# Kernel tuning notes

Measured on AMD Instinct MI355X. Metric: run time of the kernel, lower is better.

## Reference

```python
import jax, jax.numpy as jnp
import numpy as np

D_MODEL = 1024
NUM_HEADS = 16
D_K = D_MODEL // NUM_HEADS
B, S = 2, 2048


def setup_inputs() -> dict:
    key = jax.random.key(0)
    ks = jax.random.split(key, 12)
    s = 1.0 / np.sqrt(D_MODEL)
    inp = {
        "Q": jax.random.normal(ks[0], (B, S, D_MODEL), jnp.float32),
        "K": jax.random.normal(ks[1], (B, S, D_MODEL), jnp.float32),
        "V": jax.random.normal(ks[2], (B, S, D_MODEL), jnp.float32),
        "mask": jnp.tril(jnp.ones((S, S), jnp.int32))[None, None],  # causal [1,1,S,S]
        "W_Q": jax.random.uniform(ks[3], (D_MODEL, D_MODEL), jnp.float32, -s, s),
        "b_Q": jax.random.uniform(ks[4], (D_MODEL,), jnp.float32, -s, s),
        "W_K": jax.random.uniform(ks[5], (D_MODEL, D_MODEL), jnp.float32, -s, s),
        "b_K": jax.random.uniform(ks[6], (D_MODEL,), jnp.float32, -s, s),
        "W_V": jax.random.uniform(ks[7], (D_MODEL, D_MODEL), jnp.float32, -s, s),
        "b_V": jax.random.uniform(ks[8], (D_MODEL,), jnp.float32, -s, s),
        "W_O": jax.random.uniform(ks[9], (D_MODEL, D_MODEL), jnp.float32, -s, s),
        "b_O": jax.random.uniform(ks[10], (D_MODEL,), jnp.float32, -s, s),
    }
    return inp


def _split_heads(x):
    b, s, _ = x.shape
    return x.reshape(b, s, NUM_HEADS, D_K).transpose(0, 2, 1, 3)  # [B,H,S,d_k]


def reference(Q, K, V, mask, W_Q, b_Q, W_K, b_K, W_V, b_V, W_O, b_O):
    q = _split_heads(Q @ W_Q.T + b_Q)
    k = _split_heads(K @ W_K.T + b_K)
    v = _split_heads(V @ W_V.T + b_V)
    scores = jnp.einsum("bhqd,bhkd->bhqk", q, k) / jnp.sqrt(jnp.float32(D_K))
    scores = jnp.where(mask == 0, -jnp.inf, scores)
    attn = jax.nn.softmax(scores, axis=-1)
    out = jnp.einsum("bhqk,bhkd->bhqd", attn, v)
    out = out.transpose(0, 2, 1, 3).reshape(Q.shape[0], Q.shape[1], D_MODEL)
    out = out @ W_O.T + b_O
    return out, attn
```

## Files before the change

### kernel.cpp

```cpp
#include <hip/hip_runtime.h>

typedef __attribute__((ext_vector_type(4))) float f32x4;
typedef __attribute__((ext_vector_type(8))) __bf16 bf16x8;
typedef __attribute__((ext_vector_type(4))) __bf16 bf16x4;

#define D_MODEL 1024
#define S_LEN 2048
#define MROWS 4096

#if __has_builtin(__builtin_amdgcn_exp2f)
#define EXP2F(x) __builtin_amdgcn_exp2f(x)
#else
#define EXP2F(x) exp2f(x)
#endif
#if __has_builtin(__builtin_amdgcn_logf)
#define LOG2F(x) __builtin_amdgcn_logf(x)
#else
#define LOG2F(x) log2f(x)
#endif

#define QSCALE 0.1803368801111204f

__device__ __forceinline__ void gload_lds16(const void* g, void* l) {
  __builtin_amdgcn_global_load_lds(
      (const __attribute__((address_space(1))) unsigned int*)g,
      (__attribute__((address_space(3))) unsigned int*)l, 16, 0, 0);
}

__global__ void cvt_qkv(const float* __restrict__ Q, const float* __restrict__ K,
                        const float* __restrict__ V, __bf16* __restrict__ dst) {
  const int y = blockIdx.y;
  const float* src = (y == 0) ? Q : (y == 1) ? K : V;
  __bf16* d = dst + (size_t)y * (MROWS * D_MODEL);
  const int n4 = MROWS * D_MODEL / 4;
  for (int i = blockIdx.x * blockDim.x + threadIdx.x; i < n4; i += 512 * 256) {
    f32x4 v = *(const f32x4*)(src + i * 4);
    bf16x4 o;
#pragma unroll
    for (int j = 0; j < 4; ++j) o[j] = (__bf16)v[j];
    *(bf16x4*)(d + i * 4) = o;
  }
}

__global__ void cvt_w(const float* __restrict__ w0, const float* __restrict__ w1,
                      const float* __restrict__ w2, const float* __restrict__ w3,
                      __bf16* __restrict__ dst) {
  const int y = blockIdx.y;
  const float* src = (y == 0) ? w0 : (y == 1) ? w1 : (y == 2) ? w2 : w3;
  const float sc = (y == 0) ? QSCALE : 1.0f;
  __bf16* d = dst + (size_t)y * (D_MODEL * D_MODEL);
  const int n4 = D_MODEL * D_MODEL / 4;
  for (int i = blockIdx.x * blockDim.x + threadIdx.x; i < n4; i += 256 * 256) {
    f32x4 v = *(const f32x4*)(src + i * 4);
    bf16x4 o;
#pragma unroll
    for (int j = 0; j < 4; ++j) o[j] = (__bf16)(v[j] * sc);
    *(bf16x4*)(d + i * 4) = o;
  }
}

__device__ __forceinline__ void gemm_core64(const __bf16* __restrict__ A,
                                            const __bf16* __restrict__ B,
                                            __bf16* As, __bf16* Bs,
                                            int m0, int n0, f32x4 (&acc)[4][4]) {
  const int tid = threadIdx.x;
  const int lane = tid & 63, wid = tid >> 6;
  const int li = lane & 15, g = lane >> 4;
  const int wr = wid >> 1, wc = wid & 1;
  const int srow = tid >> 3, sc = tid & 7;
  const int scol = (sc ^ (srow & 7)) * 8;
  const int sw = li & 7;
  for (int k0 = 0; k0 < D_MODEL; k0 += 64) {
#pragma unroll
    for (int i = 0; i < 4; ++i) {
      const int r = i * 32 + srow;
      gload_lds16(A + (size_t)(m0 + r) * D_MODEL + k0 + scol, (char*)As + i * 4096 + wid * 1024);
      gload_lds16(B + (size_t)(n0 + r) * D_MODEL + k0 + scol, (char*)Bs + i * 4096 + wid * 1024);
    }
    __syncthreads();
#pragma unroll
    for (int kk = 0; kk < 2; ++kk) {
      bf16x8 af[4], bfr[4];
#pragma unroll
      for (int i = 0; i < 4; ++i) {
        af[i]  = *(const bf16x8*)&As[(wr * 64 + i * 16 + li) * 64 + (((kk * 4 + g) ^ sw) * 8)];
        bfr[i] = *(const bf16x8*)&Bs[(wc * 64 + i * 16 + li) * 64 + (((kk * 4 + g) ^ sw) * 8)];
      }
      __builtin_amdgcn_s_setprio(1);
#pragma unroll
      for (int i = 0; i < 4; ++i)
#pragma unroll
        for (int j = 0; j < 4; ++j)
          acc[i][j] = __builtin_amdgcn_mfma_f32_16x16x32_bf16(af[i], bfr[j], acc[i][j], 0, 0, 0);
      __builtin_amdgcn_s_setprio(0);
    }
    __syncthreads();
  }
}

__global__ __launch_bounds__(256) void qkv_gemm(
    const __bf16* __restrict__ Qb, const __bf16* __restrict__ Kb, const __bf16* __restrict__ Vb,
    const __bf16* __restrict__ Wq, const __bf16* __restrict__ Wk, const __bf16* __restrict__ Wv,
    const float* __restrict__ bq, const float* __restrict__ bk, const float* __restrict__ bv,
    __bf16* __restrict__ qp, __bf16* __restrict__ kp, __bf16* __restrict__ vt) {
  __shared__ __bf16 As[128 * 64];
  __shared__ __bf16 Bs[128 * 64];
  const int z = blockIdx.z;
  const __bf16* A = (z == 0) ? Qb : (z == 1) ? Kb : Vb;
  const __bf16* B = (z == 0) ? Wq : (z == 1) ? Wk : Wv;
  const float* bias = (z == 0) ? bq : (z == 1) ? bk : bv;
  const float bsc = (z == 0) ? QSCALE : 1.0f;
  const int m0 = blockIdx.x * 128, n0 = blockIdx.y * 128;
  f32x4 acc[4][4] = {};
  gemm_core64(A, B, As, Bs, m0, n0, acc);

  const int lane = threadIdx.x & 63, wid = threadIdx.x >> 6;
  const int li = lane & 15, g = lane >> 4;
  const int wr = wid >> 1, wc = wid & 1;
#pragma unroll
  for (int j = 0; j < 4; ++j) {
    const int n = n0 + wc * 64 + j * 16 + li;
    const float bv_ = bias[n] * bsc;
#pragma unroll
    for (int i = 0; i < 4; ++i) {
#pragma unroll
      for (int r = 0; r < 4; ++r) {
        const int m = m0 + wr * 64 + i * 16 + g * 4 + r;
        const float v = acc[i][j][r] + bv_;
        if (z == 2) {
          const int bb = m >> 11, s = m & 2047;
          vt[((size_t)(bb * D_MODEL + n)) * S_LEN + s] = (__bf16)v;
        } else {
          __bf16* o = (z == 0) ? qp : kp;
          o[(size_t)m * D_MODEL + n] = (__bf16)v;
        }
      }
    }
  }
}

__global__ __launch_bounds__(256) void o_gemm(const __bf16* __restrict__ ctx,
                                              const __bf16* __restrict__ Wo,
                                              const float* __restrict__ bo,
                                              float* __restrict__ out) {
  __shared__ __bf16 As[128 * 64];
  __shared__ __bf16 Bs[128 * 64];
  const int m0 = blockIdx.x * 128, n0 = blockIdx.y * 128;
  f32x4 acc[4][4] = {};
  gemm_core64(ctx, Wo, As, Bs, m0, n0, acc);

  const int lane = threadIdx.x & 63, wid = threadIdx.x >> 6;
  const int li = lane & 15, g = lane >> 4;
  const int wr = wid >> 1, wc = wid & 1;
#pragma unroll
  for (int j = 0; j < 4; ++j) {
    const int n = n0 + wc * 64 + j * 16 + li;
    const float bv_ = bo[n];
#pragma unroll
    for (int i = 0; i < 4; ++i)
#pragma unroll
      for (int r = 0; r < 4; ++r) {
        const int m = m0 + wr * 64 + i * 16 + g * 4 + r;
        out[(size_t)m * D_MODEL + n] = acc[i][j][r] + bv_;
      }
  }
}

__global__ __launch_bounds__(256) void attn_fused2(const __bf16* __restrict__ qp,
                                                   const __bf16* __restrict__ kp,
                                                   const __bf16* __restrict__ vt,
                                                   float* __restrict__ attn,
                                                   __bf16* __restrict__ ctx) {
  const int bid = blockIdx.x;
  const int qt = 31 - (bid >> 5);
  const int bh = bid & 31;
  const int b = bh >> 4, h = bh & 15;
  const int tid = threadIdx.x, lane = tid & 63, wid = tid >> 6;
  const int li = lane & 15, g = lane >> 4;
  const int sw = li & 7;
  const int qrow0 = qt * 64 + wid * 16;
  const float NEG_INF = -__builtin_inff();

  __shared__ __bf16 k_lds[2][64 * 64];
  __shared__ __bf16 v_lds[2][64 * 64];
  __shared__ __bf16 p_lds[4][16 * 64];

  const __bf16* qbase = qp + ((size_t)(b * S_LEN + qrow0 + li)) * D_MODEL + h * 64 + g * 8;
  const bf16x8 qf0 = *(const bf16x8*)qbase;
  const bf16x8 qf1 = *(const bf16x8*)(qbase + 32);

  const int srow = tid >> 3;
  const int sc = tid & 7;
  const int schunk = (sc ^ (srow & 7)) * 8;
  const __bf16* kpb = kp + (size_t)(b * S_LEN) * D_MODEL + h * 64 + schunk;
  const __bf16* vpb = vt + (size_t)(bh * 64) * S_LEN + schunk;

  auto stage_k = [&](int kt, int bufi) {
#pragma unroll
    for (int i = 0; i < 2; ++i)
      gload_lds16(kpb + (size_t)(kt * 64 + i * 32 + srow) * D_MODEL,
                  (char*)k_lds[bufi] + i * 4096 + wid * 1024);
  };
  auto stage_v = [&](int kt, int bufi) {
#pragma unroll
    for (int i = 0; i < 2; ++i)
      gload_lds16(vpb + (size_t)(i * 32 + srow) * S_LEN + kt * 64,
                  (char*)v_lds[bufi] + i * 4096 + wid * 1024);
  };
  auto qk_tile = [&](const __bf16* kb, f32x4 (&sv)[4]) {
    __builtin_amdgcn_s_setprio(1);
#pragma unroll
    for (int sub = 0; sub < 4; ++sub) {
      const __bf16* rp = kb + (sub * 16 + li) * 64;
      const bf16x8 k0 = *(const bf16x8*)(rp + ((g ^ sw) * 8));
      const bf16x8 k1 = *(const bf16x8*)(rp + (((4 + g) ^ sw) * 8));
      f32x4 t = {};
      t = __builtin_amdgcn_mfma_f32_16x16x32_bf16(qf0, k0, t, 0, 0, 0);
      t = __builtin_amdgcn_mfma_f32_16x16x32_bf16(qf1, k1, t, 0, 0, 0);
      sv[sub] = t;
    }
    __builtin_amdgcn_s_setprio(0);
  };

  float m_[4], l_[4];
#pragma unroll
  for (int r = 0; r < 4; ++r) { m_[r] = NEG_INF; l_[r] = 0.f; }

  int buf = 0;
  stage_k(0, 0);
  for (int kt = 0; kt <= qt; ++kt) {
    __syncthreads();
    stage_k(kt + 1, buf ^ 1);
    f32x4 sv[4];
    qk_tile(k_lds[buf], sv);
    if (kt == qt) {
      const int rowl = wid * 16 + g * 4;
#pragma unroll
      for (int sub = 0; sub < 4; ++sub) {
        const int coll = sub * 16 + li;
#pragma unroll
        for (int r = 0; r < 4; ++r)
          if (coll > rowl + r) sv[sub][r] = NEG_INF;
      }
    }
#pragma unroll
    for (int r = 0; r < 4; ++r) {
      const float v0 = sv[0][r], v1 = sv[1][r], v2 = sv[2][r], v3 = sv[3][r];
      float tm = fmaxf(fmaxf(v0, v1), fmaxf(v2, v3));
      tm = fmaxf(tm, __shfl_xor(tm, 1));
      tm = fmaxf(tm, __shfl_xor(tm, 2));
      tm = fmaxf(tm, __shfl_xor(tm, 4));
      tm = fmaxf(tm, __shfl_xor(tm, 8));
      const float mn = fmaxf(m_[r], tm);
      float e = (EXP2F(v0 - mn) + EXP2F(v1 - mn)) + (EXP2F(v2 - mn) + EXP2F(v3 - mn));
      e += __shfl_xor(e, 1);
      e += __shfl_xor(e, 2);
      e += __shfl_xor(e, 4);
      e += __shfl_xor(e, 8);
      l_[r] = l_[r] * EXP2F(m_[r] - mn) + e;
      m_[r] = mn;
    }
    buf ^= 1;
  }

  float c_[4];
#pragma unroll
  for (int r = 0; r < 4; ++r) c_[r] = m_[r] + LOG2F(l_[r]);

  float* attn_bh = attn + (size_t)bh * S_LEN * S_LEN;
  float* arp[4];
#pragma unroll
  for (int r = 0; r < 4; ++r)
    arp[r] = attn_bh + (size_t)(qrow0 + g * 4 + r) * S_LEN + li;

  __bf16* pw = &p_lds[wid][0];
  f32x4 acc[4] = {};

  __syncthreads();
  buf = 0;
  stage_k(0, 0);
  stage_v(0, 0);
  for (int kt = 0; kt <= qt; ++kt) {
    __syncthreads();
    stage_k(kt + 1, buf ^ 1);
    stage_v(kt + 1, buf ^ 1);
    f32x4 sv[4];
    qk_tile(k_lds[buf], sv);
    if (kt == qt) {
      const int rowl = wid * 16 + g * 4;
#pragma unroll
      for (int sub = 0; sub < 4; ++sub) {
        const int coll = sub * 16 + li;
#pragma unroll
        for (int r = 0; r < 4; ++r)
          if (coll > rowl + r) sv[sub][r] = NEG_INF;
      }
    }
    const int colbase = kt * 64;
#pragma unroll
    for (int r = 0; r < 4; ++r) {
      const int prow = g * 4 + r;
#pragma unroll
      for (int sub = 0; sub < 4; ++sub) {
        const float p = EXP2F(sv[sub][r] - c_[r]);
        arp[r][colbase + sub * 16] = p;
        pw[prow * 64 + (((sub * 2 + (li >> 3)) ^ (prow & 7)) * 8) + (li & 7)] = (__bf16)p;
      }
    }
    __builtin_amdgcn_s_setprio(1);
    const bf16x8 pa0 = *(const bf16x8*)&pw[li * 64 + ((g ^ sw) * 8)];
    const bf16x8 pa1 = *(const bf16x8*)&pw[li * 64 + (((4 + g) ^ sw) * 8)];
    const __bf16* vb = v_lds[buf];
#pragma unroll
    for (int c4 = 0; c4 < 4; ++c4) {
      const __bf16* vrp = vb + (c4 * 16 + li) * 64;
      const bf16x8 vf0 = *(const bf16x8*)(vrp + ((g ^ sw) * 8));
      const bf16x8 vf1 = *(const bf16x8*)(vrp + (((4 + g) ^ sw) * 8));
      acc[c4] = __builtin_amdgcn_mfma_f32_16x16x32_bf16(pa0, vf0, acc[c4], 0, 0, 0);
      acc[c4] = __builtin_amdgcn_mfma_f32_16x16x32_bf16(pa1, vf1, acc[c4], 0, 0, 0);
    }
    __builtin_amdgcn_s_setprio(0);
    buf ^= 1;
  }

#pragma unroll
  for (int c4 = 0; c4 < 4; ++c4)
#pragma unroll
    for (int r = 0; r < 4; ++r)
      ctx[((size_t)(b * S_LEN) + qrow0 + g * 4 + r) * D_MODEL + h * 64 + c4 * 16 + li] =
          (__bf16)acc[c4][r];

  const int c0 = (qt + 1) * 64;
  for (int r = 0; r < 16; ++r) {
    float* rowp = attn_bh + (size_t)(qrow0 + r) * S_LEN;
    for (int col = c0 + lane * 4; col < S_LEN; col += 256) {
      f32x4 z = {};
      *(f32x4*)(rowp + col) = z;
    }
  }
}

extern "C" void kernel_launch(void* const* d_in, const int* in_sizes, int n_in,
                              void* d_out, int out_size, void* d_ws, size_t ws_size,
                              hipStream_t stream) {
  const float* Q  = (const float*)d_in[0];
  const float* K  = (const float*)d_in[1];
  const float* V  = (const float*)d_in[2];
  const float* W_Q = (const float*)d_in[4];
  const float* b_Q = (const float*)d_in[5];
  const float* W_K = (const float*)d_in[6];
  const float* b_K = (const float*)d_in[7];
  const float* W_V = (const float*)d_in[8];
  const float* b_V = (const float*)d_in[9];
  const float* W_O = (const float*)d_in[10];
  const float* b_O = (const float*)d_in[11];

  char* ws = (char*)d_ws;
  __bf16* Qb  = (__bf16*)(ws + 0);
  __bf16* Wq  = (__bf16*)(ws + 25165824);
  __bf16* qp  = (__bf16*)(ws + 33554432);
  __bf16* kp  = (__bf16*)(ws + 41943040);
  __bf16* vtb = (__bf16*)(ws + 50331648);
  __bf16* ctx = (__bf16*)(ws + 58720256);
  __bf16* Kb = Qb + (size_t)MROWS * D_MODEL;
  __bf16* Vb = Kb + (size_t)MROWS * D_MODEL;
  __bf16* Wk = Wq + (size_t)D_MODEL * D_MODEL;
  __bf16* Wv = Wk + (size_t)D_MODEL * D_MODEL;
  __bf16* Wo = Wv + (size_t)D_MODEL * D_MODEL;

  float* out = (float*)d_out;
  float* attn = out + (size_t)MROWS * D_MODEL;

  cvt_qkv<<<dim3(512, 3), 256, 0, stream>>>(Q, K, V, Qb);
  cvt_w<<<dim3(256, 4), 256, 0, stream>>>(W_Q, W_K, W_V, W_O, Wq);

  qkv_gemm<<<dim3(32, 8, 3), 256, 0, stream>>>(Qb, Kb, Vb, Wq, Wk, Wv,
                                               b_Q, b_K, b_V, qp, kp, vtb);

  attn_fused2<<<1024, 256, 0, stream>>>(qp, kp, vtb, attn, ctx);

  o_gemm<<<dim3(32, 8), 256, 0, stream>>>(ctx, Wo, b_O, out);
}
```

Before: 247.6 us.

## Transpose score tiles per lane and drop online max in fused attention

Swaps the MFMA operands in the QK product so that each lane owns one query row and four consecutive key columns. Probabilities can then be written to the attention output as contiguous float4 stores and to LDS as bf16x4 chunks, with a new swizzle for the P buffer. The first pass drops the running max and rescaling and just sums exp2 of the raw scores, needing only two cross-lane shuffles, then multiplies by the reciprocal sum in the second pass. This removes shuffle-heavy reductions and scattered scalar stores. The cost is that softmax without max subtraction can overflow or lose precision when scores are large.

```diff
diff --git a/kernel.cpp b/kernel.cpp
--- a/kernel.cpp
+++ b/kernel.cpp
@@ -12,11 +12,6 @@
 #define EXP2F(x) __builtin_amdgcn_exp2f(x)
 #else
 #define EXP2F(x) exp2f(x)
-#endif
-#if __has_builtin(__builtin_amdgcn_logf)
-#define LOG2F(x) __builtin_amdgcn_logf(x)
-#else
-#define LOG2F(x) log2f(x)
 #endif
 
 #define QSCALE 0.1803368801111204f
@@ -166,7 +161,7 @@
   }
 }
 
-__global__ __launch_bounds__(256) void attn_fused2(const __bf16* __restrict__ qp,
+__global__ __launch_bounds__(256) void attn_fused3(const __bf16* __restrict__ qp,
                                                    const __bf16* __restrict__ kp,
                                                    const __bf16* __restrict__ vt,
                                                    float* __restrict__ attn,
@@ -207,25 +202,23 @@
       gload_lds16(vpb + (size_t)(i * 32 + srow) * S_LEN + kt * 64,
                   (char*)v_lds[bufi] + i * 4096 + wid * 1024);
   };
-  auto qk_tile = [&](const __bf16* kb, f32x4 (&sv)[4]) {
+  auto qk_tile = [&](const __bf16* kb_, f32x4 (&sv)[4]) {
     __builtin_amdgcn_s_setprio(1);
 #pragma unroll
-    for (int sub = 0; sub < 4; ++sub) {
-      const __bf16* rp = kb + (sub * 16 + li) * 64;
+    for (int kb = 0; kb < 4; ++kb) {
+      const __bf16* rp = kb_ + (kb * 16 + li) * 64;
       const bf16x8 k0 = *(const bf16x8*)(rp + ((g ^ sw) * 8));
       const bf16x8 k1 = *(const bf16x8*)(rp + (((4 + g) ^ sw) * 8));
       f32x4 t = {};
-      t = __builtin_amdgcn_mfma_f32_16x16x32_bf16(qf0, k0, t, 0, 0, 0);
-      t = __builtin_amdgcn_mfma_f32_16x16x32_bf16(qf1, k1, t, 0, 0, 0);
-      sv[sub] = t;
+      t = __builtin_amdgcn_mfma_f32_16x16x32_bf16(k0, qf0, t, 0, 0, 0);
+      t = __builtin_amdgcn_mfma_f32_16x16x32_bf16(k1, qf1, t, 0, 0, 0);
+      sv[kb] = t;
     }
     __builtin_amdgcn_s_setprio(0);
   };
-
-  float m_[4], l_[4];
-#pragma unroll
-  for (int r = 0; r < 4; ++r) { m_[r] = NEG_INF; l_[r] = 0.f; }
-
+  const int ql = wid * 16 + li;
+
+  float lsum = 0.f;
   int buf = 0;
   stage_k(0, 0);
   for (int kt = 0; kt <= qt; ++kt) {
@@ -234,46 +227,26 @@
     f32x4 sv[4];
     qk_tile(k_lds[buf], sv);
     if (kt == qt) {
-      const int rowl = wid * 16 + g * 4;
-#pragma unroll
-      for (int sub = 0; sub < 4; ++sub) {
-        const int coll = sub * 16 + li;
+#pragma unroll
+      for (int kb = 0; kb < 4; ++kb)
 #pragma unroll
         for (int r = 0; r < 4; ++r)
-          if (coll > rowl + r) sv[sub][r] = NEG_INF;
-      }
-    }
-#pragma unroll
-    for (int r = 0; r < 4; ++r) {
-      const float v0 = sv[0][r], v1 = sv[1][r], v2 = sv[2][r], v3 = sv[3][r];
-      float tm = fmaxf(fmaxf(v0, v1), fmaxf(v2, v3));
-      tm = fmaxf(tm, __shfl_xor(tm, 1));
-      tm = fmaxf(tm, __shfl_xor(tm, 2));
-      tm = fmaxf(tm, __shfl_xor(tm, 4));
-      tm = fmaxf(tm, __shfl_xor(tm, 8));
-      const float mn = fmaxf(m_[r], tm);
-      float e = (EXP2F(v0 - mn) + EXP2F(v1 - mn)) + (EXP2F(v2 - mn) + EXP2F(v3 - mn));
-      e += __shfl_xor(e, 1);
-      e += __shfl_xor(e, 2);
-      e += __shfl_xor(e, 4);
-      e += __shfl_xor(e, 8);
-      l_[r] = l_[r] * EXP2F(m_[r] - mn) + e;
-      m_[r] = mn;
-    }
+          if (kb * 16 + g * 4 + r > ql) sv[kb][r] = NEG_INF;
+    }
+    float e[4];
+#pragma unroll
+    for (int kb = 0; kb < 4; ++kb)
+      e[kb] = (EXP2F(sv[kb][0]) + EXP2F(sv[kb][1])) + (EXP2F(sv[kb][2]) + EXP2F(sv[kb][3]));
+    lsum += (e[0] + e[1]) + (e[2] + e[3]);
     buf ^= 1;
   }
-
-  float c_[4];
-#pragma unroll
-  for (int r = 0; r < 4; ++r) c_[r] = m_[r] + LOG2F(l_[r]);
-
-  float* attn_bh = attn + (size_t)bh * S_LEN * S_LEN;
-  float* arp[4];
-#pragma unroll
-  for (int r = 0; r < 4; ++r)
-    arp[r] = attn_bh + (size_t)(qrow0 + g * 4 + r) * S_LEN + li;
-
+  lsum += __shfl_xor(lsum, 16);
+  lsum += __shfl_xor(lsum, 32);
+  const float inv_l = 1.f / lsum;
+
+  float* attn_row = attn + (size_t)bh * S_LEN * S_LEN + (size_t)(qt * 64 + ql) * S_LEN;
   __bf16* pw = &p_lds[wid][0];
+  const int e8 = (li & 7) << 1;
   f32x4 acc[4] = {};
 
   __syncthreads();
@@ -287,29 +260,27 @@
     f32x4 sv[4];
     qk_tile(k_lds[buf], sv);
     if (kt == qt) {
-      const int rowl = wid * 16 + g * 4;
-#pragma unroll
-      for (int sub = 0; sub < 4; ++sub) {
-        const int coll = sub * 16 + li;
+#pragma unroll
+      for (int kb = 0; kb < 4; ++kb)
 #pragma unroll
         for (int r = 0; r < 4; ++r)
-          if (coll > rowl + r) sv[sub][r] = NEG_INF;
+          if (kb * 16 + g * 4 + r > ql) sv[kb][r] = NEG_INF;
+    }
+#pragma unroll
+    for (int kb = 0; kb < 4; ++kb) {
+      f32x4 p;
+      bf16x4 pb;
+#pragma unroll
+      for (int r = 0; r < 4; ++r) {
+        p[r] = EXP2F(sv[kb][r]) * inv_l;
+        pb[r] = (__bf16)p[r];
       }
-    }
-    const int colbase = kt * 64;
-#pragma unroll
-    for (int r = 0; r < 4; ++r) {
-      const int prow = g * 4 + r;
-#pragma unroll
-      for (int sub = 0; sub < 4; ++sub) {
-        const float p = EXP2F(sv[sub][r] - c_[r]);
-        arp[r][colbase + sub * 16] = p;
-        pw[prow * 64 + (((sub * 2 + (li >> 3)) ^ (prow & 7)) * 8) + (li & 7)] = (__bf16)p;
-      }
+      *(f32x4*)(attn_row + kt * 64 + kb * 16 + g * 4) = p;
+      *(bf16x4*)&pw[li * 64 + (((kb * 4 + g) ^ e8) * 4)] = pb;
     }
     __builtin_amdgcn_s_setprio(1);
-    const bf16x8 pa0 = *(const bf16x8*)&pw[li * 64 + ((g ^ sw) * 8)];
-    const bf16x8 pa1 = *(const bf16x8*)&pw[li * 64 + (((4 + g) ^ sw) * 8)];
+    const bf16x8 pa0 = *(const bf16x8*)&pw[li * 64 + (((2 * g) ^ e8) * 4)];
+    const bf16x8 pa1 = *(const bf16x8*)&pw[li * 64 + (((8 + 2 * g) ^ e8) * 4)];
     const __bf16* vb = v_lds[buf];
 #pragma unroll
     for (int c4 = 0; c4 < 4; ++c4) {
@@ -330,6 +301,7 @@
       ctx[((size_t)(b * S_LEN) + qrow0 + g * 4 + r) * D_MODEL + h * 64 + c4 * 16 + li] =
           (__bf16)acc[c4][r];
 
+  float* attn_bh = attn + (size_t)bh * S_LEN * S_LEN;
   const int c0 = (qt + 1) * 64;
   for (int r = 0; r < 16; ++r) {
     float* rowp = attn_bh + (size_t)(qrow0 + r) * S_LEN;
@@ -377,7 +349,7 @@
   qkv_gemm<<<dim3(32, 8, 3), 256, 0, stream>>>(Qb, Kb, Vb, Wq, Wk, Wv,
                                                b_Q, b_K, b_V, qp, kp, vtb);
 
-  attn_fused2<<<1024, 256, 0, stream>>>(qp, kp, vtb, attn, ctx);
+  attn_fused3<<<1024, 256, 0, stream>>>(qp, kp, vtb, attn, ctx);
 
   o_gemm<<<dim3(32, 8), 256, 0, stream>>>(ctx, Wo, b_O, out);
 }
```

After: 266.5 us. 7.7% more time.

## Widen attention blocks to 128 query rows and drop online softmax max

Applied to the files above, without the earlier changes.

The attention kernel now uses 512-thread blocks covering 128 query rows. Eight waves share each staged 64-key K/V tile, which halves the global-to-LDS traffic per query row and the number of blocks. Waves in the lower half idle for one tile on the diagonal. The first pass no longer tracks a running max: it sums exp2 of raw scores and reduces across lanes once at the end, then normalises by a reciprocal. This removes per-tile shuffles and rescaling, but it can overflow for inputs whose scores are large.

```diff
diff --git a/kernel.cpp b/kernel.cpp
--- a/kernel.cpp
+++ b/kernel.cpp
@@ -12,11 +12,6 @@
 #define EXP2F(x) __builtin_amdgcn_exp2f(x)
 #else
 #define EXP2F(x) exp2f(x)
-#endif
-#if __has_builtin(__builtin_amdgcn_logf)
-#define LOG2F(x) __builtin_amdgcn_logf(x)
-#else
-#define LOG2F(x) log2f(x)
 #endif
 
 #define QSCALE 0.1803368801111204f
@@ -166,24 +161,24 @@
   }
 }
 
-__global__ __launch_bounds__(256) void attn_fused2(const __bf16* __restrict__ qp,
-                                                   const __bf16* __restrict__ kp,
-                                                   const __bf16* __restrict__ vt,
-                                                   float* __restrict__ attn,
-                                                   __bf16* __restrict__ ctx) {
+__global__ __launch_bounds__(512, 4) void attn_fused4(const __bf16* __restrict__ qp,
+                                                      const __bf16* __restrict__ kp,
+                                                      const __bf16* __restrict__ vt,
+                                                      float* __restrict__ attn,
+                                                      __bf16* __restrict__ ctx) {
   const int bid = blockIdx.x;
-  const int qt = 31 - (bid >> 5);
+  const int qt = 15 - (bid >> 5);
   const int bh = bid & 31;
   const int b = bh >> 4, h = bh & 15;
   const int tid = threadIdx.x, lane = tid & 63, wid = tid >> 6;
   const int li = lane & 15, g = lane >> 4;
   const int sw = li & 7;
-  const int qrow0 = qt * 64 + wid * 16;
+  const int qrow0 = qt * 128 + wid * 16;
   const float NEG_INF = -__builtin_inff();
 
   __shared__ __bf16 k_lds[2][64 * 64];
   __shared__ __bf16 v_lds[2][64 * 64];
-  __shared__ __bf16 p_lds[4][16 * 64];
+  __shared__ __bf16 p_lds[8][16 * 64];
 
   const __bf16* qbase = qp + ((size_t)(b * S_LEN + qrow0 + li)) * D_MODEL + h * 64 + g * 8;
   const bf16x8 qf0 = *(const bf16x8*)qbase;
@@ -196,16 +191,10 @@
   const __bf16* vpb = vt + (size_t)(bh * 64) * S_LEN + schunk;
 
   auto stage_k = [&](int kt, int bufi) {
-#pragma unroll
-    for (int i = 0; i < 2; ++i)
-      gload_lds16(kpb + (size_t)(kt * 64 + i * 32 + srow) * D_MODEL,
-                  (char*)k_lds[bufi] + i * 4096 + wid * 1024);
+    gload_lds16(kpb + (size_t)(kt * 64 + srow) * D_MODEL, (char*)k_lds[bufi] + wid * 1024);
   };
   auto stage_v = [&](int kt, int bufi) {
-#pragma unroll
-    for (int i = 0; i < 2; ++i)
-      gload_lds16(vpb + (size_t)(i * 32 + srow) * S_LEN + kt * 64,
-                  (char*)v_lds[bufi] + i * 4096 + wid * 1024);
+    gload_lds16(vpb + (size_t)srow * S_LEN + kt * 64, (char*)v_lds[bufi] + wid * 1024);
   };
   auto qk_tile = [&](const __bf16* kb, f32x4 (&sv)[4]) {
     __builtin_amdgcn_s_setprio(1);
@@ -222,50 +211,44 @@
     __builtin_amdgcn_s_setprio(0);
   };
 
-  float m_[4], l_[4];
-#pragma unroll
-  for (int r = 0; r < 4; ++r) { m_[r] = NEG_INF; l_[r] = 0.f; }
-
+  const int ktmax_w = 2 * qt + ((wid >= 4) ? 1 : 0);
+  const int kt_end = 2 * qt + 1;
+
+  float esum[4] = {0.f, 0.f, 0.f, 0.f};
   int buf = 0;
   stage_k(0, 0);
-  for (int kt = 0; kt <= qt; ++kt) {
+  for (int kt = 0; kt <= kt_end; ++kt) {
     __syncthreads();
     stage_k(kt + 1, buf ^ 1);
-    f32x4 sv[4];
-    qk_tile(k_lds[buf], sv);
-    if (kt == qt) {
-      const int rowl = wid * 16 + g * 4;
-#pragma unroll
-      for (int sub = 0; sub < 4; ++sub) {
-        const int coll = sub * 16 + li;
-#pragma unroll
-        for (int r = 0; r < 4; ++r)
-          if (coll > rowl + r) sv[sub][r] = NEG_INF;
-      }
-    }
-#pragma unroll
-    for (int r = 0; r < 4; ++r) {
-      const float v0 = sv[0][r], v1 = sv[1][r], v2 = sv[2][r], v3 = sv[3][r];
-      float tm = fmaxf(fmaxf(v0, v1), fmaxf(v2, v3));
-      tm = fmaxf(tm, __shfl_xor(tm, 1));
-      tm = fmaxf(tm, __shfl_xor(tm, 2));
-      tm = fmaxf(tm, __shfl_xor(tm, 4));
-      tm = fmaxf(tm, __shfl_xor(tm, 8));
-      const float mn = fmaxf(m_[r], tm);
-      float e = (EXP2F(v0 - mn) + EXP2F(v1 - mn)) + (EXP2F(v2 - mn) + EXP2F(v3 - mn));
-      e += __shfl_xor(e, 1);
-      e += __shfl_xor(e, 2);
-      e += __shfl_xor(e, 4);
-      e += __shfl_xor(e, 8);
-      l_[r] = l_[r] * EXP2F(m_[r] - mn) + e;
-      m_[r] = mn;
+    if (kt <= ktmax_w) {
+      f32x4 sv[4];
+      qk_tile(k_lds[buf], sv);
+      if (kt == ktmax_w) {
+        const int rowl = qrow0 + g * 4;
+#pragma unroll
+        for (int sub = 0; sub < 4; ++sub) {
+          const int col = kt * 64 + sub * 16 + li;
+#pragma unroll
+          for (int r = 0; r < 4; ++r)
+            if (col > rowl + r) sv[sub][r] = NEG_INF;
+        }
+      }
+#pragma unroll
+      for (int r = 0; r < 4; ++r)
+        esum[r] += (EXP2F(sv[0][r]) + EXP2F(sv[1][r])) + (EXP2F(sv[2][r]) + EXP2F(sv[3][r]));
     }
     buf ^= 1;
   }
-
-  float c_[4];
-#pragma unroll
-  for (int r = 0; r < 4; ++r) c_[r] = m_[r] + LOG2F(l_[r]);
+  float inv_l[4];
+#pragma unroll
+  for (int r = 0; r < 4; ++r) {
+    float e = esum[r];
+    e += __shfl_xor(e, 1);
+    e += __shfl_xor(e, 2);
+    e += __shfl_xor(e, 4);
+    e += __shfl_xor(e, 8);
+    inv_l[r] = 1.f / e;
+  }
 
   float* attn_bh = attn + (size_t)bh * S_LEN * S_LEN;
   float* arp[4];
@@ -280,46 +263,48 @@
   buf = 0;
   stage_k(0, 0);
   stage_v(0, 0);
-  for (int kt = 0; kt <= qt; ++kt) {
+  for (int kt = 0; kt <= kt_end; ++kt) {
     __syncthreads();
     stage_k(kt + 1, buf ^ 1);
     stage_v(kt + 1, buf ^ 1);
-    f32x4 sv[4];
-    qk_tile(k_lds[buf], sv);
-    if (kt == qt) {
-      const int rowl = wid * 16 + g * 4;
-#pragma unroll
-      for (int sub = 0; sub < 4; ++sub) {
-        const int coll = sub * 16 + li;
-#pragma unroll
-        for (int r = 0; r < 4; ++r)
-          if (coll > rowl + r) sv[sub][r] = NEG_INF;
-      }
-    }
-    const int colbase = kt * 64;
-#pragma unroll
-    for (int r = 0; r < 4; ++r) {
-      const int prow = g * 4 + r;
-#pragma unroll
-      for (int sub = 0; sub < 4; ++sub) {
-        const float p = EXP2F(sv[sub][r] - c_[r]);
-        arp[r][colbase + sub * 16] = p;
-        pw[prow * 64 + (((sub * 2 + (li >> 3)) ^ (prow & 7)) * 8) + (li & 7)] = (__bf16)p;
-      }
-    }
-    __builtin_amdgcn_s_setprio(1);
-    const bf16x8 pa0 = *(const bf16x8*)&pw[li * 64 + ((g ^ sw) * 8)];
-    const bf16x8 pa1 = *(const bf16x8*)&pw[li * 64 + (((4 + g) ^ sw) * 8)];
-    const __bf16* vb = v_lds[buf];
-#pragma unroll
-    for (int c4 = 0; c4 < 4; ++c4) {
-      const __bf16* vrp = vb + (c4 * 16 + li) * 64;
-      const bf16x8 vf0 = *(const bf16x8*)(vrp + ((g ^ sw) * 8));
-      const bf16x8 vf1 = *(const bf16x8*)(vrp + (((4 + g) ^ sw) * 8));
-      acc[c4] = __builtin_amdgcn_mfma_f32_16x16x32_bf16(pa0, vf0, acc[c4], 0, 0, 0);
-      acc[c4] = __builtin_amdgcn_mfma_f32_16x16x32_bf16(pa1, vf1, acc[c4], 0, 0, 0);
-    }
-    __builtin_amdgcn_s_setprio(0);
+    if (kt <= ktmax_w) {
+      f32x4 sv[4];
+      qk_tile(k_lds[buf], sv);
+      if (kt == ktmax_w) {
+        const int rowl = qrow0 + g * 4;
+#pragma unroll
+        for (int sub = 0; sub < 4; ++sub) {
+          const int col = kt * 64 + sub * 16 + li;
+#pragma unroll
+          for (int r = 0; r < 4; ++r)
+            if (col > rowl + r) sv[sub][r] = NEG_INF;
+        }
+      }
+      const int colbase = kt * 64;
+#pragma unroll
+      for (int r = 0; r < 4; ++r) {
+        const int prow = g * 4 + r;
+#pragma unroll
+        for (int sub = 0; sub < 4; ++sub) {
+          const float p = EXP2F(sv[sub][r]) * inv_l[r];
+          arp[r][colbase + sub * 16] = p;
+          pw[prow * 64 + (((sub * 2 + (li >> 3)) ^ (prow & 7)) * 8) + (li & 7)] = (__bf16)p;
+        }
+      }
+      __builtin_amdgcn_s_setprio(1);
+      const bf16x8 pa0 = *(const bf16x8*)&pw[li * 64 + ((g ^ sw) * 8)];
+      const bf16x8 pa1 = *(const bf16x8*)&pw[li * 64 + (((4 + g) ^ sw) * 8)];
+      const __bf16* vb = v_lds[buf];
+#pragma unroll
+      for (int c4 = 0; c4 < 4; ++c4) {
+        const __bf16* vrp = vb + (c4 * 16 + li) * 64;
+        const bf16x8 vf0 = *(const bf16x8*)(vrp + ((g ^ sw) * 8));
+        const bf16x8 vf1 = *(const bf16x8*)(vrp + (((4 + g) ^ sw) * 8));
+        acc[c4] = __builtin_amdgcn_mfma_f32_16x16x32_bf16(pa0, vf0, acc[c4], 0, 0, 0);
+        acc[c4] = __builtin_amdgcn_mfma_f32_16x16x32_bf16(pa1, vf1, acc[c4], 0, 0, 0);
+      }
+      __builtin_amdgcn_s_setprio(0);
+    }
     buf ^= 1;
   }
 
@@ -330,7 +315,7 @@
       ctx[((size_t)(b * S_LEN) + qrow0 + g * 4 + r) * D_MODEL + h * 64 + c4 * 16 + li] =
           (__bf16)acc[c4][r];
 
-  const int c0 = (qt + 1) * 64;
+  const int c0 = (ktmax_w + 1) * 64;
   for (int r = 0; r < 16; ++r) {
     float* rowp = attn_bh + (size_t)(qrow0 + r) * S_LEN;
     for (int col = c0 + lane * 4; col < S_LEN; col += 256) {
@@ -377,7 +362,7 @@
   qkv_gemm<<<dim3(32, 8, 3), 256, 0, stream>>>(Qb, Kb, Vb, Wq, Wk, Wv,
                                                b_Q, b_K, b_V, qp, kp, vtb);
 
-  attn_fused2<<<1024, 256, 0, stream>>>(qp, kp, vtb, attn, ctx);
+  attn_fused4<<<512, 512, 0, stream>>>(qp, kp, vtb, attn, ctx);
 
   o_gemm<<<dim3(32, 8), 256, 0, stream>>>(ctx, Wo, b_O, out);
 }
```

Result: slower. 253.8 us (+2.5%).
